# Performance work log

Measured on AMD Instinct MI355X. Metric: run time of the kernel, lower is better.

The kernel has to match this reference:

```python
import jax, jax.numpy as jnp
import numpy as np

B, T, E = 32, 100, 512
H = 640          # predictor embed/hidden dim
J = 640          # joint hidden dim
V = 4096         # vocab size; blank index == V
BLANK = V
MAX_SYMBOLS = 2  # max_symbols_per_step


def setup_inputs() -> dict:
    key = jax.random.key(0)
    ks = jax.random.split(key, 11)
    s = 0.02
    return {
        "encoder_output": jax.random.normal(ks[0], (B, E, T), jnp.float32),
        "encoded_lengths": jax.random.randint(ks[1], (B,), 0, T).astype(jnp.int32),
        "embed": jax.random.normal(ks[2], (V + 1, H), jnp.float32) * s,
        "W_i": jax.random.normal(ks[3], (H, 4 * H), jnp.float32) * s,
        "W_h": jax.random.normal(ks[4], (H, 4 * H), jnp.float32) * s,
        "b_lstm": jnp.zeros((4 * H,), jnp.float32),
        "W_enc": jax.random.normal(ks[5], (E, J), jnp.float32) * s,
        "W_pred": jax.random.normal(ks[6], (H, J), jnp.float32) * s,
        "b_joint": jnp.zeros((J,), jnp.float32),
        "W_out": jax.random.normal(ks[7], (J, V + 1), jnp.float32) * s,
        "b_out": jnp.zeros((V + 1,), jnp.float32),
    }


def _lstm_step(x, h, c, W_i, W_h, b):
    z = x @ W_i + h @ W_h + b                      # [B, 4H]
    i, f, g, o = jnp.split(z, 4, axis=-1)
    i, f, o = jax.nn.sigmoid(i), jax.nn.sigmoid(f), jax.nn.sigmoid(o)
    c = f * c + i * jnp.tanh(g)
    return o * jnp.tanh(c), c


def _greedy_decode(enc_bte, lengths, embed, W_i, W_h, b_lstm,
                   W_enc, W_pred, b_joint, W_out, b_out):
    """Batched RNNT greedy decode. Returns (labels [B,T*MS], counts [B], score [B]).
    Instead of the host-side early break when blank_mask is all-true, we run the
    bounded inner loop with per-sequence commit masking; once a sequence is blank
    its state/label/output freeze, so the per-sequence results are identical."""
    Bv = enc_bte.shape[0]
    enc_proj = enc_bte @ W_enc                     # [B, T, J] (same math as per-step enc projection)
    batch_ix = jnp.arange(Bv)

    h0 = jnp.zeros((Bv, H), enc_bte.dtype)
    c0 = jnp.zeros((Bv, H), enc_bte.dtype)
    last0 = jnp.full((Bv,), BLANK, jnp.int32)      # SOS == blank
    labels0 = jnp.full((Bv, T * MAX_SYMBOLS), BLANK, jnp.int32)
    counts0 = jnp.zeros((Bv,), jnp.int32)
    score0 = jnp.zeros((Bv,), jnp.float32)

    def inner(icarry, s_and_t):
        h, c, last_label, blank_mask, labels, counts, score = icarry
        s, t = s_and_t
        use_sos = jnp.logical_and(t == 0, s == 0)
        x = jnp.where(use_sos, 0.0, embed[last_label])      # [B, H]; SOS -> zero vector
        h1, c1 = _lstm_step(x, h, c, W_i, W_h, b_lstm)
        logits = jax.nn.relu(enc_proj[:, t] + h1 @ W_pred + b_joint) @ W_out + b_out  # [B, V+1]
        logp = jax.nn.log_softmax(logits, axis=-1)          # CPU path in original
        k = jnp.argmax(logp, axis=-1)                       # [B]
        v = jnp.take_along_axis(logp, k[:, None], axis=-1)[:, 0]
        new_blank = blank_mask | (k == BLANK)
        commit = ~new_blank                                  # only non-blank sequences advance
        cm = commit[:, None]
        h = jnp.where(cm, h1, h)
        c = jnp.where(cm, c1, c)
        k32 = k.astype(jnp.int32)
        last_label = jnp.where(commit, k32, last_label)
        labels = labels.at[batch_ix, counts].set(
            jnp.where(commit, k32, labels[batch_ix, counts]))
        counts = counts + commit.astype(jnp.int32)
        score = score + jnp.where(commit, v, 0.0)
        return (h, c, last_label, new_blank, labels, counts, score), None

    def outer(carry, t):
        h, c, last_label, labels, counts, score = carry
        blank_mask = t >= lengths                            # [B]
        icarry = (h, c, last_label, blank_mask, labels, counts, score)
        icarry, _ = jax.lax.scan(
            lambda cc, s: inner(cc, (s, t)), icarry, jnp.arange(MAX_SYMBOLS))
        h, c, last_label, _, labels, counts, score = icarry
        return (h, c, last_label, labels, counts, score), None

    carry = (h0, c0, last0, labels0, counts0, score0)
    carry, _ = jax.lax.scan(outer, carry, jnp.arange(T))
    _, _, _, labels, counts, score = carry
    return labels, counts, score


def reference(encoder_output, encoded_lengths, embed, W_i, W_h, b_lstm,
              W_enc, W_pred, b_joint, W_out, b_out):
    enc = jnp.transpose(encoder_output, (0, 2, 1))           # (B, F, T) -> (B, T, F)
    labels, counts, score = _greedy_decode(
        enc, encoded_lengths, embed, W_i, W_h, b_lstm,
        W_enc, W_pred, b_joint, W_out, b_out)
    return labels, counts, score
```

## Files before the change

kernel.cpp:

```cpp
#include <hip/hip_runtime.h>


#define NB 512
#define S1B 320
#define HRS 20480

__device__ __forceinline__ unsigned f2ord(float f) {
  unsigned u = __float_as_uint(f);
  return (u & 0x80000000u) ? ~u : (u | 0x80000000u);
}
__device__ __forceinline__ float ord2f(unsigned u) {
  return __uint_as_float((u & 0x80000000u) ? (u & 0x7fffffffu) : ~u);
}
__device__ __forceinline__ unsigned long long shfl_xor_u64(unsigned long long x, int m) {
  int lo = __shfl_xor((int)(unsigned)x, m, 64);
  int hi = __shfl_xor((int)(unsigned)(x >> 32), m, 64);
  return ((unsigned long long)(unsigned)hi << 32) | (unsigned)lo;
}

__device__ __forceinline__ void st_coh_f32(float* p, float v) {
  asm volatile("global_store_dword %0, %1, off sc0 sc1" :: "v"(p), "v"(v) : "memory");
}
__device__ __forceinline__ void st_coh_u32(unsigned* p, unsigned v) {
  asm volatile("global_store_dword %0, %1, off sc0 sc1" :: "v"(p), "v"(v) : "memory");
}
__device__ __forceinline__ unsigned ld_coh_u32(const unsigned* p) {
  unsigned r;
  asm volatile("global_load_dword %0, %1, off sc0 sc1\n\ts_waitcnt vmcnt(0)"
               : "=v"(r) : "v"(p) : "memory");
  return r;
}
__device__ __forceinline__ bool poll2(const unsigned* p1, const unsigned* p2,
                                      unsigned it) {
  unsigned r1, r2;
  asm volatile("global_load_dword %0, %2, off sc0 sc1\n\t"
               "global_load_dword %1, %3, off sc0 sc1\n\t"
               "s_waitcnt vmcnt(0)"
               : "=v"(r1), "=v"(r2) : "v"(p1), "v"(p2) : "memory");
  return (r1 >= it) && (r2 >= it);
}

__device__ __forceinline__ void gbarrier(unsigned* __restrict__ arrive,
                                         unsigned* __restrict__ go, unsigned it) {
  const int blk = blockIdx.x, tid = threadIdx.x;
  __syncthreads();
  if (blk == 0) {
    int f1 = 1 + tid; if (f1 > 511) f1 = 511;
    int f2 = 257 + tid; if (f2 > 511) f2 = 511;
    while (!poll2(arrive + f1 * 4, arrive + f2 * 4, it))
      __builtin_amdgcn_s_sleep(1);
    __syncthreads();
    if (tid < 64) st_coh_u32(go + tid * 4, it);
    __syncthreads();
  } else {
    if (tid == 0) {
      st_coh_u32(arrive + blk * 4, it);
      while (ld_coh_u32(go + (blk & 63) * 4) < it) __builtin_amdgcn_s_sleep(1);
    }
    __syncthreads();
  }
}

__device__ __forceinline__ void stage_tile(float (*__restrict__ t)[160],
                                           const float* __restrict__ src_row,
                                           int rb, int q) {
#pragma unroll
  for (int p = 0; p < 5; ++p) {
    int c = q + (p << 3);
    float4 v = *(const float4*)(src_row + (c << 2));
    *(float4*)&t[rb][(c ^ (rb & 7)) << 2] = v;
  }
}
__device__ __forceinline__ float4 tile_read(const float (*__restrict__ t)[160],
                                            int b, int c) {
  return *(const float4*)&t[b][(c ^ (b & 7)) << 2];
}

__global__ __launch_bounds__(256) void rnnt_prep(
    const float* __restrict__ enc, const float* __restrict__ W_i,
    const float* __restrict__ W_h, const float* __restrict__ W_pred,
    const float* __restrict__ W_out, const float* __restrict__ W_enc,
    const float* __restrict__ b_joint,
    float* __restrict__ out, float* __restrict__ Wcat_t,
    float* __restrict__ Wpred_t, float* __restrict__ Wout_t,
    float* __restrict__ enc_projB, float* __restrict__ h_ring,
    unsigned long long* __restrict__ kslot, unsigned long long* __restrict__ sslot,
    unsigned* __restrict__ arrive, unsigned* __restrict__ go) {
  const int blk = blockIdx.x, tid = threadIdx.x;
  const int gtid = blk * 256 + tid;
  const int GT = gridDim.x * 256;
  __shared__ float s_tr[32][33];

  for (int x = gtid; x < 6464; x += GT) out[x] = (x < 6400) ? 4096.0f : 0.0f;
  for (int x = gtid; x < HRS; x += GT) h_ring[(size_t)200 * HRS + x] = 0.f;
  for (int x = gtid; x < 51200; x += GT) { kslot[x] = 0ull; sslot[x] = 0ull; }
  for (int x = gtid; x < NB * 4; x += GT) arrive[x] = 0u;
  for (int x = gtid; x < 64 * 4; x += GT) go[x] = 0u;

  {
    const int NT0 = 1600, NT1 = 1600, NT2 = 400, NT3 = 2580;
    for (int tl = blk; tl < NT0 + NT1 + NT2 + NT3; tl += gridDim.x) {
      const float* src; float* dst; int C, DS, DO, CT; int tt = tl;
      if (tt < NT0)               { src = W_i;    dst = Wcat_t;  C = 2560; DS = 1280; DO = 0;   CT = 80; }
      else if ((tt -= NT0) < NT1) { src = W_h;    dst = Wcat_t;  C = 2560; DS = 1280; DO = 640; CT = 80; }
      else if ((tt -= NT1) < NT2) { src = W_pred; dst = Wpred_t; C = 640;  DS = 640;  DO = 0;   CT = 20; }
      else { tt -= NT2;             src = W_out;  dst = Wout_t;  C = 4097; DS = 640;  DO = 0;   CT = 129; }
      int rt = tt / CT, ct = tt % CT;
      int r0 = rt * 32, c0 = ct * 32;
      __syncthreads();
#pragma unroll
      for (int p = 0; p < 4; ++p) {
        int rr = (tid >> 5) + 8 * p, cc = tid & 31;
        float v = 0.f;
        if (c0 + cc < C) v = src[(r0 + rr) * C + c0 + cc];
        s_tr[rr][cc] = v;
      }
      __syncthreads();
#pragma unroll
      for (int p = 0; p < 4; ++p) {
        int cc2 = (tid >> 5) + 8 * p, rr2 = tid & 31;
        if (c0 + cc2 < C) dst[(c0 + cc2) * DS + DO + r0 + rr2] = s_tr[rr2][cc2];
      }
    }
  }

  for (int idx = gtid; idx < 2048000; idx += GT) {
    int b = idx / 64000, r = idx % 64000;
    int tt = r / 640, j = r % 640;
    const float* ep = enc + b * 51200;
    float acc = b_joint[j];
#pragma unroll 4
    for (int e = 0; e < 512; ++e) acc += ep[e * 100 + tt] * W_enc[e * 640 + j];
    enc_projB[idx] = acc;
  }
}

__global__ __launch_bounds__(256, 2) void rnnt_decode(
    const int* __restrict__ lens, const float* __restrict__ embed,
    const float* __restrict__ b_lstm, const float* __restrict__ b_out,
    float* __restrict__ out,
    const float* __restrict__ Wcat_t, const float* __restrict__ Wpred_t,
    const float* __restrict__ Wout_t, const float* __restrict__ enc_projB,
    float* __restrict__ h_ring, float* __restrict__ jt_ring,
    unsigned long long* __restrict__ kslot, unsigned long long* __restrict__ sslot,
    unsigned* __restrict__ arrive, unsigned* __restrict__ go) {
  const int blk = blockIdx.x, tid = threadIdx.x;

  __shared__ float s_tile[32][160];
  __shared__ float s_wout[9 * 640];
  __shared__ float s_zp[2][4][32][2];
  __shared__ float s_red[4][64];
  __shared__ unsigned long long s_dk[32], s_ds[32];
  __shared__ int s_last[32], s_hsrc[32], s_commit[32];

  for (int x = tid; x < 9 * 160; x += 256) {
    int col = x / 160, cc = x - col * 160;
    int vcol = (col < 8) ? blk * 8 + col : 4096;
    *(float4*)&s_wout[col * 640 + cc * 4] =
        *(const float4*)(Wout_t + (size_t)vcol * 640 + cc * 4);
  }

  int last_r = 4096, hsrc_r = 200, cnt_r = 0;
  bool blank_r = false;
  float score_r = 0.f;
  float c_comm = 0.f, c_cand = 0.f;
  unsigned it = 0;
  const int len_b = lens[tid & 31];

  for (int i = 0;; ++i) {
    if (i > 0) {
      int ip = i - 1;
      int b8 = tid >> 3, sl = tid & 7;
      unsigned long long kv = kslot[((size_t)ip * 32 + b8) * 8 + sl];
      unsigned long long sv = sslot[((size_t)ip * 32 + b8) * 8 + sl];
#pragma unroll
      for (int d = 1; d < 8; d <<= 1) {
        unsigned long long ok = shfl_xor_u64(kv, d);
        if (ok > kv) kv = ok;
        sv += shfl_xor_u64(sv, d);
      }
      if (sl == 0) { s_dk[b8] = kv; s_ds[b8] = sv; }
    }
    __syncthreads();
    if (tid < 32) {
      int b = tid;
      int cm = 0;
      if (i > 0) {
        unsigned long long key = s_dk[b], sum = s_ds[b];
        int kArg = 4096 - (int)(key & 0xffffffffu);
        float bl = ord2f((unsigned)(key >> 32));
        float lse = logf((float)sum * 0x1p-32f);
        float vsc = bl - lse;
        int im1 = i - 1, tp = im1 >> 1, sp = im1 & 1;
        bool blank_in = (sp == 0) ? (tp >= len_b) : blank_r;
        bool nb = blank_in || (kArg == 4096);
        blank_r = nb;
        if (!nb) {
          if (blk == b) out[b * 200 + cnt_r] = (float)kArg;
          last_r = kArg; hsrc_r = im1; cnt_r++; score_r += vsc; cm = 1;
        }
      }
      if (i == 200 && blk == b) { out[6400 + b] = (float)cnt_r; out[6432 + b] = score_r; }
      s_last[b] = last_r; s_hsrc[b] = hsrc_r; s_commit[b] = cm;
    }
    __syncthreads();
    if (i == 200) return;
    const int t = i >> 1;

    if (blk < S1B) {
      const int b = tid & 31;
      const int g = (tid >> 5) & 3;
      const int half = tid >> 7;
      const int j0 = blk * 2;
      float a0 = 0.f, a1 = 0.f, a2 = 0.f, a3 = 0.f;
      float e0 = 0.f, e1 = 0.f, e2 = 0.f, e3 = 0.f;
      if (i > 0) {
        const int rb = tid >> 3, q = tid & 7;
#pragma unroll 1
        for (int tt = 0; tt < 8; ++tt) {
          const float* src = (tt < 4)
              ? embed + (size_t)s_last[rb] * 640 + tt * 160
              : h_ring + (size_t)s_hsrc[rb] * HRS + rb * 640 + (tt - 4) * 160;
          stage_tile(s_tile, src, rb, q);
          __syncthreads();
          if ((tt >> 2) == half) {
            const float* wr = Wcat_t + (size_t)(g * 640 + j0) * 1280 +
                              half * 640 + (tt & 3) * 160;
            const float* wr2 = wr + 1280;
#pragma unroll 8
            for (int cc = 0; cc < 40; ++cc) {
              float4 xv = tile_read(s_tile, b, cc);
              float4 wa = *(const float4*)(wr + cc * 4);
              float4 wb = *(const float4*)(wr2 + cc * 4);
              a0 += wa.x * xv.x; a1 += wa.y * xv.y;
              a2 += wa.z * xv.z; a3 += wa.w * xv.w;
              e0 += wb.x * xv.x; e1 += wb.y * xv.y;
              e2 += wb.z * xv.z; e3 += wb.w * xv.w;
            }
          }
          __syncthreads();
        }
      }
      float z0 = (a0 + a1) + (a2 + a3);
      float z1 = (e0 + e1) + (e2 + e3);
      if (half == 0) { z0 += b_lstm[g * 640 + j0]; z1 += b_lstm[g * 640 + j0 + 1]; }
      s_zp[half][g][b][0] = z0;
      s_zp[half][g][b][1] = z1;
    }
    __syncthreads();
    if (blk < S1B && tid < 64) {
      const int b = tid >> 1, j_l = tid & 1;
      float zi = s_zp[0][0][b][j_l] + s_zp[1][0][b][j_l];
      float zf = s_zp[0][1][b][j_l] + s_zp[1][1][b][j_l];
      float zg = s_zp[0][2][b][j_l] + s_zp[1][2][b][j_l];
      float zo = s_zp[0][3][b][j_l] + s_zp[1][3][b][j_l];
      if (s_commit[b]) c_comm = c_cand;
      float ig = 1.f / (1.f + expf(-zi));
      float fg = 1.f / (1.f + expf(-zf));
      float og = 1.f / (1.f + expf(-zo));
      float cn = fg * c_comm + ig * tanhf(zg);
      float hn = og * tanhf(cn);
      c_cand = cn;
      st_coh_f32(&h_ring[(size_t)i * HRS + b * 640 + blk * 2 + j_l], hn);
    }
    gbarrier(arrive, go, ++it);

    if (blk < S1B) {
      const int w = tid >> 6, lane = tid & 63, bb = lane >> 1, j_l = lane & 1;
      const int j = blk * 2 + j_l;
      const int rb = tid >> 3, q = tid & 7;
      float r0 = 0.f, r1 = 0.f, r2 = 0.f, r3 = 0.f;
#pragma unroll 1
      for (int tt = 0; tt < 4; ++tt) {
        const float* src = h_ring + (size_t)i * HRS + rb * 640 + tt * 160;
        stage_tile(s_tile, src, rb, q);
        __syncthreads();
        if (w == tt) {
          const float* wp = Wpred_t + (size_t)j * 640 + w * 160;
#pragma unroll 8
          for (int cc = 0; cc < 40; ++cc) {
            float4 hv = tile_read(s_tile, bb, cc);
            float4 wv = *(const float4*)(wp + cc * 4);
            r0 += wv.x * hv.x; r1 += wv.y * hv.y;
            r2 += wv.z * hv.z; r3 += wv.w * hv.w;
          }
        }
        __syncthreads();
      }
      s_red[w][lane] = (r0 + r1) + (r2 + r3);
    }
    __syncthreads();
    if (blk < S1B && tid < 64) {
      const int b = tid >> 1, j_l = tid & 1, j = blk * 2 + j_l;
      float sm = (s_red[0][tid] + s_red[1][tid]) + (s_red[2][tid] + s_red[3][tid]);
      float val = enc_projB[(b * 100 + t) * 640 + j] + sm;
      st_coh_f32(&jt_ring[(size_t)i * HRS + b * 640 + j], fmaxf(val, 0.f));
    }
    gbarrier(arrive, go, ++it);

    {
      const int b = tid >> 3, v_l = tid & 7;
      const int v = blk * 8 + v_l;
      const int kq = v_l;
      float a0 = 0.f, a1 = 0.f, a2 = 0.f, a3 = 0.f;
      float p0 = 0.f, p1 = 0.f, p2 = 0.f, p3 = 0.f;
      const int rb = tid >> 3, q = tid & 7;
#pragma unroll 1
      for (int tt = 0; tt < 4; ++tt) {
        const float* src = jt_ring + (size_t)i * HRS + rb * 640 + tt * 160;
        stage_tile(s_tile, src, rb, q);
        __syncthreads();
        const float* wk = s_wout + v_l * 640 + tt * 160;
#pragma unroll 8
        for (int cc = 0; cc < 40; ++cc) {
          float4 jv = tile_read(s_tile, b, cc);
          float4 wv = *(const float4*)(wk + cc * 4);
          a0 += wv.x * jv.x; a1 += wv.y * jv.y;
          a2 += wv.z * jv.z; a3 += wv.w * jv.w;
        }
        if (blk == NB - 1 && (kq >> 1) == tt) {
          const float* wb4 = s_wout + 8 * 640 + kq * 80;
          const int c0 = (kq & 1) * 20;
#pragma unroll
          for (int cc = 0; cc < 20; ++cc) {
            float4 jv = tile_read(s_tile, b, c0 + cc);
            float4 wv = *(const float4*)(wb4 + cc * 4);
            p0 += wv.x * jv.x; p1 += wv.y * jv.y;
            p2 += wv.z * jv.z; p3 += wv.w * jv.w;
          }
        }
        __syncthreads();
      }
      float acc = ((a0 + a1) + (a2 + a3)) + b_out[v];
      unsigned long long key =
          ((unsigned long long)f2ord(acc) << 32) | (unsigned)(4096 - v);
      unsigned long long isum =
          (unsigned long long)(expf(acc) * 4294967296.0f + 0.5f);
#pragma unroll
      for (int d = 1; d < 8; d <<= 1) {
        unsigned long long ok = shfl_xor_u64(key, d);
        if (ok > key) key = ok;
        isum += shfl_xor_u64(isum, d);
      }
      if (v_l == 0) {
        atomicMax(&kslot[((size_t)i * 32 + b) * 8 + (blk & 7)], key);
        atomicAdd(&sslot[((size_t)i * 32 + b) * 8 + (blk & 7)], isum);
      }
      if (blk == NB - 1) {
        float part = (p0 + p1) + (p2 + p3);
#pragma unroll
        for (int d = 1; d < 8; d <<= 1) part += __shfl_xor(part, d, 64);
        if (kq == 0) {
          float aB = part + b_out[4096];
          unsigned long long key2 = ((unsigned long long)f2ord(aB) << 32);
          unsigned long long is2 =
              (unsigned long long)(expf(aB) * 4294967296.0f + 0.5f);
          atomicMax(&kslot[((size_t)i * 32 + b) * 8 + 7], key2);
          atomicAdd(&sslot[((size_t)i * 32 + b) * 8 + 7], is2);
        }
      }
    }
    gbarrier(arrive, go, ++it);
  }
}

extern "C" void kernel_launch(void* const* d_in, const int* in_sizes, int n_in,
                              void* d_out, int out_size, void* d_ws, size_t ws_size,
                              hipStream_t stream) {
  (void)in_sizes; (void)n_in; (void)out_size; (void)ws_size;
  const float* enc    = (const float*)d_in[0];
  const int*   lens   = (const int*)d_in[1];
  const float* embed  = (const float*)d_in[2];
  const float* W_i    = (const float*)d_in[3];
  const float* W_h    = (const float*)d_in[4];
  const float* b_lstm = (const float*)d_in[5];
  const float* W_enc  = (const float*)d_in[6];
  const float* W_pred = (const float*)d_in[7];
  const float* b_joint= (const float*)d_in[8];
  const float* W_out  = (const float*)d_in[9];
  const float* b_out  = (const float*)d_in[10];
  float* out = (float*)d_out;

  char* ws = (char*)d_ws;
  size_t off = 0;
  auto carve = [&](size_t bytes) -> void* {
    void* p = ws + off;
    off += (bytes + 255) & ~(size_t)255;
    return p;
  };
  unsigned* arrive           = (unsigned*)carve((size_t)NB * 4 * 4);
  unsigned* go               = (unsigned*)carve((size_t)64 * 4 * 4);
  unsigned long long* kslot  = (unsigned long long*)carve((size_t)51200 * 8);
  unsigned long long* sslot  = (unsigned long long*)carve((size_t)51200 * 8);
  float* h_ring   = (float*)carve((size_t)201 * HRS * 4);
  float* jt_ring  = (float*)carve((size_t)200 * HRS * 4);
  float* Wpred_t  = (float*)carve((size_t)640 * 640 * 4);
  float* Wcat_t   = (float*)carve((size_t)2560 * 1280 * 4);
  float* Wout_t   = (float*)carve((size_t)4097 * 640 * 4);
  float* enc_projB= (float*)carve((size_t)32 * 100 * 640 * 4);

  rnnt_prep<<<2048, 256, 0, stream>>>(
      enc, W_i, W_h, W_pred, W_out, W_enc, b_joint,
      out, Wcat_t, Wpred_t, Wout_t, enc_projB, h_ring, kslot, sslot, arrive, go);
  rnnt_decode<<<NB, 256, 0, stream>>>(
      lens, embed, b_lstm, b_out, out,
      Wcat_t, Wpred_t, Wout_t, enc_projB, h_ring, jt_ring, kslot, sslot,
      arrive, go);
}
```

Before: 15.66 ms.

## Prefetch next staging tile into registers and pad barrier flags to separate lines

Replaces the synchronous global-to-LDS tile staging in the LSTM, predictor and joint-output loops with register double-buffering, so the global loads for the next chunk are issued before the current chunk's compute. Spreads the grid-barrier arrive and go flags to larger strides so each flag sits in its own cache line, and lengthens the sleep on the go poll. Pads the LDS W_out rows to 644 floats to reduce bank conflicts and reads the blank column directly from global memory instead of LDS. The cost is more registers per thread, which could hurt occupancy under launch_bounds(256,2), and a larger flag workspace.

```diff
diff --git a/kernel.cpp b/kernel.cpp
--- a/kernel.cpp
+++ b/kernel.cpp
@@ -4,6 +4,8 @@
 #define NB 512
 #define S1B 320
 #define HRS 20480
+#define ARRS 64
+#define GOS 256
 
 __device__ __forceinline__ unsigned f2ord(float f) {
   unsigned u = __float_as_uint(f);
@@ -47,30 +49,20 @@
   if (blk == 0) {
     int f1 = 1 + tid; if (f1 > 511) f1 = 511;
     int f2 = 257 + tid; if (f2 > 511) f2 = 511;
-    while (!poll2(arrive + f1 * 4, arrive + f2 * 4, it))
+    while (!poll2(arrive + f1 * ARRS, arrive + f2 * ARRS, it))
       __builtin_amdgcn_s_sleep(1);
     __syncthreads();
-    if (tid < 64) st_coh_u32(go + tid * 4, it);
+    if (tid < 64) st_coh_u32(go + tid * GOS, it);
     __syncthreads();
   } else {
     if (tid == 0) {
-      st_coh_u32(arrive + blk * 4, it);
-      while (ld_coh_u32(go + (blk & 63) * 4) < it) __builtin_amdgcn_s_sleep(1);
+      st_coh_u32(arrive + blk * ARRS, it);
+      while (ld_coh_u32(go + (blk & 63) * GOS) < it) __builtin_amdgcn_s_sleep(4);
     }
     __syncthreads();
   }
 }
 
-__device__ __forceinline__ void stage_tile(float (*__restrict__ t)[160],
-                                           const float* __restrict__ src_row,
-                                           int rb, int q) {
-#pragma unroll
-  for (int p = 0; p < 5; ++p) {
-    int c = q + (p << 3);
-    float4 v = *(const float4*)(src_row + (c << 2));
-    *(float4*)&t[rb][(c ^ (rb & 7)) << 2] = v;
-  }
-}
 __device__ __forceinline__ float4 tile_read(const float (*__restrict__ t)[160],
                                             int b, int c) {
   return *(const float4*)&t[b][(c ^ (b & 7)) << 2];
@@ -94,8 +86,8 @@
   for (int x = gtid; x < 6464; x += GT) out[x] = (x < 6400) ? 4096.0f : 0.0f;
   for (int x = gtid; x < HRS; x += GT) h_ring[(size_t)200 * HRS + x] = 0.f;
   for (int x = gtid; x < 51200; x += GT) { kslot[x] = 0ull; sslot[x] = 0ull; }
-  for (int x = gtid; x < NB * 4; x += GT) arrive[x] = 0u;
-  for (int x = gtid; x < 64 * 4; x += GT) go[x] = 0u;
+  for (int x = gtid; x < NB * ARRS; x += GT) arrive[x] = 0u;
+  for (int x = gtid; x < 64 * GOS; x += GT) go[x] = 0u;
 
   {
     const int NT0 = 1600, NT1 = 1600, NT2 = 400, NT3 = 2580;
@@ -147,17 +139,16 @@
   const int blk = blockIdx.x, tid = threadIdx.x;
 
   __shared__ float s_tile[32][160];
-  __shared__ float s_wout[9 * 640];
+  __shared__ float s_wout[8 * 644];
   __shared__ float s_zp[2][4][32][2];
   __shared__ float s_red[4][64];
   __shared__ unsigned long long s_dk[32], s_ds[32];
   __shared__ int s_last[32], s_hsrc[32], s_commit[32];
 
-  for (int x = tid; x < 9 * 160; x += 256) {
+  for (int x = tid; x < 8 * 160; x += 256) {
     int col = x / 160, cc = x - col * 160;
-    int vcol = (col < 8) ? blk * 8 + col : 4096;
-    *(float4*)&s_wout[col * 640 + cc * 4] =
-        *(const float4*)(Wout_t + (size_t)vcol * 640 + cc * 4);
+    *(float4*)&s_wout[col * 644 + cc * 4] =
+        *(const float4*)(Wout_t + (size_t)(blk * 8 + col) * 640 + cc * 4);
   }
 
   int last_r = 4096, hsrc_r = 200, cnt_r = 0;
@@ -166,6 +157,7 @@
   float c_comm = 0.f, c_cand = 0.f;
   unsigned it = 0;
   const int len_b = lens[tid & 31];
+  const int rb = tid >> 3, q = tid & 7;
 
   for (int i = 0;; ++i) {
     if (i > 0) {
@@ -215,13 +207,32 @@
       float a0 = 0.f, a1 = 0.f, a2 = 0.f, a3 = 0.f;
       float e0 = 0.f, e1 = 0.f, e2 = 0.f, e3 = 0.f;
       if (i > 0) {
-        const int rb = tid >> 3, q = tid & 7;
+        float4 pf0, pf1, pf2, pf3, pf4;
+        {
+          const float* s0 = embed + (size_t)s_last[rb] * 640;
+          pf0 = *(const float4*)(s0 + (q << 2));
+          pf1 = *(const float4*)(s0 + ((q + 8) << 2));
+          pf2 = *(const float4*)(s0 + ((q + 16) << 2));
+          pf3 = *(const float4*)(s0 + ((q + 24) << 2));
+          pf4 = *(const float4*)(s0 + ((q + 32) << 2));
+        }
 #pragma unroll 1
         for (int tt = 0; tt < 8; ++tt) {
-          const float* src = (tt < 4)
-              ? embed + (size_t)s_last[rb] * 640 + tt * 160
-              : h_ring + (size_t)s_hsrc[rb] * HRS + rb * 640 + (tt - 4) * 160;
-          stage_tile(s_tile, src, rb, q);
+          *(float4*)&s_tile[rb][((q)      ^ (rb & 7)) << 2] = pf0;
+          *(float4*)&s_tile[rb][((q + 8)  ^ (rb & 7)) << 2] = pf1;
+          *(float4*)&s_tile[rb][((q + 16) ^ (rb & 7)) << 2] = pf2;
+          *(float4*)&s_tile[rb][((q + 24) ^ (rb & 7)) << 2] = pf3;
+          *(float4*)&s_tile[rb][((q + 32) ^ (rb & 7)) << 2] = pf4;
+          if (tt < 7) {
+            const float* src = (tt + 1 < 4)
+                ? embed + (size_t)s_last[rb] * 640 + (tt + 1) * 160
+                : h_ring + (size_t)s_hsrc[rb] * HRS + rb * 640 + (tt - 3) * 160;
+            pf0 = *(const float4*)(src + (q << 2));
+            pf1 = *(const float4*)(src + ((q + 8) << 2));
+            pf2 = *(const float4*)(src + ((q + 16) << 2));
+            pf3 = *(const float4*)(src + ((q + 24) << 2));
+            pf4 = *(const float4*)(src + ((q + 32) << 2));
+          }
           __syncthreads();
           if ((tt >> 2) == half) {
             const float* wr = Wcat_t + (size_t)(g * 640 + j0) * 1280 +
@@ -268,12 +279,31 @@
     if (blk < S1B) {
       const int w = tid >> 6, lane = tid & 63, bb = lane >> 1, j_l = lane & 1;
       const int j = blk * 2 + j_l;
-      const int rb = tid >> 3, q = tid & 7;
       float r0 = 0.f, r1 = 0.f, r2 = 0.f, r3 = 0.f;
+      float4 pf0, pf1, pf2, pf3, pf4;
+      {
+        const float* s0 = h_ring + (size_t)i * HRS + rb * 640;
+        pf0 = *(const float4*)(s0 + (q << 2));
+        pf1 = *(const float4*)(s0 + ((q + 8) << 2));
+        pf2 = *(const float4*)(s0 + ((q + 16) << 2));
+        pf3 = *(const float4*)(s0 + ((q + 24) << 2));
+        pf4 = *(const float4*)(s0 + ((q + 32) << 2));
+      }
 #pragma unroll 1
       for (int tt = 0; tt < 4; ++tt) {
-        const float* src = h_ring + (size_t)i * HRS + rb * 640 + tt * 160;
-        stage_tile(s_tile, src, rb, q);
+        *(float4*)&s_tile[rb][((q)      ^ (rb & 7)) << 2] = pf0;
+        *(float4*)&s_tile[rb][((q + 8)  ^ (rb & 7)) << 2] = pf1;
+        *(float4*)&s_tile[rb][((q + 16) ^ (rb & 7)) << 2] = pf2;
+        *(float4*)&s_tile[rb][((q + 24) ^ (rb & 7)) << 2] = pf3;
+        *(float4*)&s_tile[rb][((q + 32) ^ (rb & 7)) << 2] = pf4;
+        if (tt < 3) {
+          const float* src = h_ring + (size_t)i * HRS + rb * 640 + (tt + 1) * 160;
+          pf0 = *(const float4*)(src + (q << 2));
+          pf1 = *(const float4*)(src + ((q + 8) << 2));
+          pf2 = *(const float4*)(src + ((q + 16) << 2));
+          pf3 = *(const float4*)(src + ((q + 24) << 2));
+          pf4 = *(const float4*)(src + ((q + 32) << 2));
+        }
         __syncthreads();
         if (w == tt) {
           const float* wp = Wpred_t + (size_t)j * 640 + w * 160;
@@ -304,13 +334,32 @@
       const int kq = v_l;
       float a0 = 0.f, a1 = 0.f, a2 = 0.f, a3 = 0.f;
       float p0 = 0.f, p1 = 0.f, p2 = 0.f, p3 = 0.f;
-      const int rb = tid >> 3, q = tid & 7;
+      float4 pf0, pf1, pf2, pf3, pf4;
+      {
+        const float* s0 = jt_ring + (size_t)i * HRS + rb * 640;
+        pf0 = *(const float4*)(s0 + (q << 2));
+        pf1 = *(const float4*)(s0 + ((q + 8) << 2));
+        pf2 = *(const float4*)(s0 + ((q + 16) << 2));
+        pf3 = *(const float4*)(s0 + ((q + 24) << 2));
+        pf4 = *(const float4*)(s0 + ((q + 32) << 2));
+      }
 #pragma unroll 1
       for (int tt = 0; tt < 4; ++tt) {
-        const float* src = jt_ring + (size_t)i * HRS + rb * 640 + tt * 160;
-        stage_tile(s_tile, src, rb, q);
+        *(float4*)&s_tile[rb][((q)      ^ (rb & 7)) << 2] = pf0;
+        *(float4*)&s_tile[rb][((q + 8)  ^ (rb & 7)) << 2] = pf1;
+        *(float4*)&s_tile[rb][((q + 16) ^ (rb & 7)) << 2] = pf2;
+        *(float4*)&s_tile[rb][((q + 24) ^ (rb & 7)) << 2] = pf3;
+        *(float4*)&s_tile[rb][((q + 32) ^ (rb & 7)) << 2] = pf4;
+        if (tt < 3) {
+          const float* src = jt_ring + (size_t)i * HRS + rb * 640 + (tt + 1) * 160;
+          pf0 = *(const float4*)(src + (q << 2));
+          pf1 = *(const float4*)(src + ((q + 8) << 2));
+          pf2 = *(const float4*)(src + ((q + 16) << 2));
+          pf3 = *(const float4*)(src + ((q + 24) << 2));
+          pf4 = *(const float4*)(src + ((q + 32) << 2));
+        }
         __syncthreads();
-        const float* wk = s_wout + v_l * 640 + tt * 160;
+        const float* wk = s_wout + v_l * 644 + tt * 160;
 #pragma unroll 8
         for (int cc = 0; cc < 40; ++cc) {
           float4 jv = tile_read(s_tile, b, cc);
@@ -319,7 +368,7 @@
           a2 += wv.z * jv.z; a3 += wv.w * jv.w;
         }
         if (blk == NB - 1 && (kq >> 1) == tt) {
-          const float* wb4 = s_wout + 8 * 640 + kq * 80;
+          const float* wb4 = Wout_t + (size_t)4096 * 640 + kq * 80;
           const int c0 = (kq & 1) * 20;
 #pragma unroll
           for (int cc = 0; cc < 20; ++cc) {
@@ -388,8 +437,8 @@
     off += (bytes + 255) & ~(size_t)255;
     return p;
   };
-  unsigned* arrive           = (unsigned*)carve((size_t)NB * 4 * 4);
-  unsigned* go               = (unsigned*)carve((size_t)64 * 4 * 4);
+  unsigned* arrive           = (unsigned*)carve((size_t)NB * ARRS * 4);
+  unsigned* go               = (unsigned*)carve((size_t)64 * GOS * 4);
   unsigned long long* kslot  = (unsigned long long*)carve((size_t)51200 * 8);
   unsigned long long* sslot  = (unsigned long long*)carve((size_t)51200 * 8);
   float* h_ring   = (float*)carve((size_t)201 * HRS * 4);
```

After: 12.76 ms. 1.23x faster.
